# Performance work log

Hardware: AMD Instinct MI355X
Metric: run time of the kernel (lower is better)

## Reference

```python
import jax, jax.numpy as jnp
import numpy as np
from jax import lax

N, D = 16384, 512
E_SPEC, E_SHARED = 8, 2


def setup_inputs() -> dict:
    key = jax.random.key(0)
    ks = jax.random.split(key, 7)
    return {
        "x": jax.random.normal(ks[0], (N, D), dtype=jnp.float32),
        "spec_router_logits": jax.random.normal(ks[1], (N, E_SPEC), dtype=jnp.float32),
        "shared_router_logits": jax.random.normal(ks[2], (N, E_SHARED), dtype=jnp.float32),
        "spec_W": jax.random.normal(ks[3], (E_SPEC, D, D), dtype=jnp.float32) * 0.02,
        "spec_b": jax.random.normal(ks[4], (E_SPEC, D), dtype=jnp.float32) * 0.02,
        "shared_W": jax.random.normal(ks[5], (E_SHARED, D, D), dtype=jnp.float32) * 0.02,
        "shared_b": jax.random.normal(ks[6], (E_SHARED, D), dtype=jnp.float32) * 0.02,
        "top_k": 2,
    }


def reference(x, spec_router_logits, shared_router_logits, spec_W, spec_b, shared_W, shared_b, top_k):
    n, e_spec = spec_router_logits.shape
    # --- specific experts: top-k routing with renormalized weights ---
    spec_probs = jax.nn.softmax(spec_router_logits, axis=1)          # [N, E_spec]
    topk_w, topk_idx = lax.top_k(spec_probs, top_k)                  # [N, K]
    topk_w = topk_w / (jnp.sum(topk_w, axis=1, keepdims=True) + 1e-6)
    # dense per-token per-expert weight matrix (zero for unselected), matching
    # the original dense mask-accumulate loop
    weights = jnp.zeros((n, e_spec), dtype=spec_probs.dtype)
    weights = weights.at[jnp.arange(n)[:, None], topk_idx].add(topk_w)  # [N, E_spec]
    # dense eval of all specific experts (Linear d->d), then weighted combine
    spec_outs = jnp.einsum('nd,edf->enf', x, spec_W) + spec_b[:, None, :]  # [E,N,D]
    spec_out = jnp.einsum('ne,enf->nf', weights, spec_outs)                # [N,D]
    # --- shared experts: soft combine over softmax probs ---
    shared_probs = jax.nn.softmax(shared_router_logits, axis=1)           # [N, E_shared]
    shared_outs = jnp.einsum('nd,edf->enf', x, shared_W) + shared_b[:, None, :]
    shared_out = jnp.einsum('ne,enf->nf', shared_probs, shared_outs)
    return spec_out + shared_out
```

## Files before the change

### kernel.cpp

```cpp
#include <hip/hip_runtime.h>
#include <stdint.h>

typedef unsigned short ushort_t;
typedef __attribute__((ext_vector_type(8))) short short8;
typedef __attribute__((ext_vector_type(4))) float f32x4;
typedef __attribute__((ext_vector_type(4))) unsigned int u32x4;

#define TOK  16384
#define DIM  512
#define NPAIR 64
#define MAXTILES 156

__device__ __forceinline__ unsigned short f2bf(float f) {
  union { float f; uint32_t u; } v; v.f = f;
  uint32_t u = v.u;
  uint32_t r = (u + 0x7fffu + ((u >> 16) & 1u)) >> 16;
  return (unsigned short)r;
}

__global__ void k_prep(const float* __restrict__ wspec, const float* __restrict__ wsh,
                       ushort_t* __restrict__ wt,
                       const float* __restrict__ sl, const float* __restrict__ shl,
                       float* __restrict__ w4, int* __restrict__ pairid,
                       int* __restrict__ cnt) {
  if (blockIdx.z < 10) {
    __shared__ float t[32][33];
    int e = blockIdx.z;
    const float* src = (e < 8) ? (wspec + e * DIM * DIM) : (wsh + (e - 8) * DIM * DIM);
    int tx = threadIdx.x, ty = threadIdx.y;
    int d = blockIdx.y * 32 + ty, f = blockIdx.x * 32 + tx;
    t[ty][tx] = src[d * DIM + f];
    __syncthreads();
    int fo = blockIdx.x * 32 + ty, dd = blockIdx.y * 32 + tx;
    wt[(size_t)e * DIM * DIM + fo * DIM + dd] = f2bf(t[tx][ty]);
    return;
  }
  int blk = blockIdx.y * 16 + blockIdx.x;
  if (blk >= 16) return;
  __shared__ int h[NPAIR];
  int tid = threadIdx.y * 32 + threadIdx.x;
  int n = blk * 1024 + tid;
  if (tid < NPAIR) h[tid] = 0;
  __syncthreads();
  float l[8];
  float m = -1e30f;
#pragma unroll
  for (int i = 0; i < 8; ++i) { l[i] = sl[n*8 + i]; m = fmaxf(m, l[i]); }
  float s = 0.f;
#pragma unroll
  for (int i = 0; i < 8; ++i) { l[i] = expf(l[i] - m); s += l[i]; }
  float inv = 1.f / s;
#pragma unroll
  for (int i = 0; i < 8; ++i) l[i] *= inv;
  int i1 = 0; float v1 = l[0];
#pragma unroll
  for (int i = 1; i < 8; ++i) if (l[i] > v1) { v1 = l[i]; i1 = i; }
  int i2 = -1; float v2 = -1.f;
#pragma unroll
  for (int i = 0; i < 8; ++i) if (i != i1 && l[i] > v2) { v2 = l[i]; i2 = i; }
  float rs = 1.f / (v1 + v2 + 1e-6f);
  float w1 = v1 * rs, w2 = v2 * rs;
  int pmin, pmax; float wa, wb;
  if (i1 < i2) { pmin = i1; pmax = i2; wa = w1; wb = w2; }
  else         { pmin = i2; pmax = i1; wa = w2; wb = w1; }
  float s0 = shl[n*2], s1 = shl[n*2 + 1];
  float mm = fmaxf(s0, s1);
  float e0 = expf(s0 - mm), e1 = expf(s1 - mm);
  float si = 1.f / (e0 + e1);
  w4[n*4 + 0] = wa;
  w4[n*4 + 1] = wb;
  w4[n*4 + 2] = e0 * si;
  w4[n*4 + 3] = e1 * si;
  int p = pmin * 8 + pmax;
  pairid[n] = p;
  atomicAdd(&h[p], 1);
  __syncthreads();
  if (tid < NPAIR && h[tid]) atomicAdd(&cnt[tid], h[tid]);
}

__global__ void k_scan(const int* __restrict__ cnt, int* __restrict__ off,
                       int* __restrict__ cursor, int* __restrict__ tsinfo,
                       int* __restrict__ tileinfo, ushort_t* __restrict__ idx) {
  int l = threadIdx.x;
  int c = cnt[l];
  int t = (c + 127) >> 7;
  int sc = c, st = t;
#pragma unroll
  for (int d = 1; d < 64; d <<= 1) {
    int vc = __shfl_up(sc, d, 64);
    int vt = __shfl_up(st, d, 64);
    if (l >= d) { sc += vc; st += vt; }
  }
  int offv = sc - c, tsv = st - t;
  off[l] = offv; cursor[l] = offv;
  if (l == 63) tsinfo[64] = st;
  for (int q = 0; q < t; ++q) tileinfo[tsv + q] = (l << 16) | q;
  for (int i = l; i < 128; i += 64) idx[TOK + i] = 0;
}

__global__ void k_fill(const int* __restrict__ pairid, int* __restrict__ cursor,
                       ushort_t* __restrict__ idx) {
  __shared__ int hcnt[NPAIR];
  __shared__ int hbase[NPAIR];
  int tid = threadIdx.x;
  int n = blockIdx.x * 256 + tid;
  if (tid < NPAIR) hcnt[tid] = 0;
  __syncthreads();
  int p = pairid[n];
  int r = atomicAdd(&hcnt[p], 1);
  __syncthreads();
  if (tid < NPAIR && hcnt[tid]) hbase[tid] = atomicAdd(&cursor[tid], hcnt[tid]);
  __syncthreads();
  idx[hbase[p] + r] = (ushort_t)n;
}

__global__ void k_gather(const float* __restrict__ x, const ushort_t* __restrict__ idx,
                         ushort_t* __restrict__ xg) {
  int row = blockIdx.x * 4 + (threadIdx.x >> 6);
  int lane = threadIdx.x & 63;
  int t = (int)idx[row];
  const float* src = x + (size_t)t * DIM + lane * 8;
  f32x4 v0 = *(const f32x4*)src;
  f32x4 v1 = *(const f32x4*)(src + 4);
  u32x4 o;
  o[0] = (uint32_t)f2bf(v0[0]) | ((uint32_t)f2bf(v0[1]) << 16);
  o[1] = (uint32_t)f2bf(v0[2]) | ((uint32_t)f2bf(v0[3]) << 16);
  o[2] = (uint32_t)f2bf(v1[0]) | ((uint32_t)f2bf(v1[1]) << 16);
  o[3] = (uint32_t)f2bf(v1[2]) | ((uint32_t)f2bf(v1[3]) << 16);
  *(u32x4*)(xg + (size_t)row * DIM + lane * 8) = o;
}

__global__ __launch_bounds__(256, 3)
void k_moe(const ushort_t* __restrict__ xg, const ushort_t* __restrict__ wt,
           const float* __restrict__ w4, const ushort_t* __restrict__ idx,
           const int* __restrict__ off, const int* __restrict__ cnt,
           const int* __restrict__ tsinfo, const int* __restrict__ tileinfo,
           const float* __restrict__ bspec, const float* __restrict__ bsh,
           float* __restrict__ out) {
  __shared__ ushort_t aB[16384];
  __shared__ ushort_t bB[8192];
  __shared__ float wLT[4 * 128];
  __shared__ float wRT[4 * 128];

  const int tid  = threadIdx.x;
  const int lane = tid & 63;
  const int w    = tid >> 6;
  const int wr   = w >> 1, wc = w & 1;

  int bx  = blockIdx.x;
  int r   = bx >> 3, cdx = bx & 7;
  if (r >= tsinfo[64]) return;
  int info = tileinfo[r];
  int p = info >> 16, tstart = info & 0xffff;
  const int base = off[p] + (tstart << 7);
  int cl = cnt[p] - (tstart << 7); if (cl > 128) cl = 128;
  const int e0 = p >> 3, e1 = p & 7;
  const int tcol = cdx << 6;

  int soffA[8];
#pragma unroll
  for (int q = 0; q < 8; ++q) {
    int pp   = (q << 12) + tid * 16;
    int row  = pp >> 8;
    int orig = (pp & 255) ^ ((row & 7) << 4);
    soffA[q] = row * DIM + (orig >> 1);
  }
  const ushort_t* aSrc = xg + (size_t)base * DIM;
  const ushort_t* bSrc = wt + (size_t)tcol * DIM;

  for (int i = tid; i < 512; i += 256) {
    int j = i >> 7, rs = i & 127;
    float wa = 1.f, wb = 1.f;
    if (rs < cl) {
      int t = (int)idx[base + rs];
      wa = w4[t * 4 + j];
      wb = w4[t * 4 + ((j + 1) & 3)];
    }
    wLT[i] = wa;
    wRT[i] = wa / wb;
  }

  int aRd[4][4], bRd[2][4];
#pragma unroll
  for (int i = 0; i < 4; ++i) {
    int row = wr * 64 + i * 16 + (lane & 15);
#pragma unroll
    for (int ksl = 0; ksl < 4; ++ksl)
      aRd[i][ksl] = row * 256 + ((((ksl << 6) + ((lane >> 4) << 4))) ^ ((row & 7) << 4));
  }
#pragma unroll
  for (int i = 0; i < 2; ++i) {
    int col = wc * 32 + i * 16 + (lane & 15);
#pragma unroll
    for (int ksl = 0; ksl < 4; ++ksl)
      bRd[i][ksl] = col * 256 + ((((ksl << 6) + ((lane >> 4) << 4))) ^ ((col & 7) << 4));
  }

  f32x4 acc[4][2];
#pragma unroll
  for (int a = 0; a < 4; ++a)
#pragma unroll
    for (int b = 0; b < 2; ++b) acc[a][b] = (f32x4){0.f, 0.f, 0.f, 0.f};

#pragma unroll 1
  for (int s = 0; s < 16; ++s) {
    int ks = s >> 2, j = s & 3;
    if (j == 0) {
#pragma unroll
      for (int q = 0; q < 8; ++q)
        __builtin_amdgcn_global_load_lds(
            (const __attribute__((address_space(1))) void*)(aSrc + (ks << 7) + soffA[q]),
            (__attribute__((address_space(3))) void*)((char*)aB + (q << 12) + tid * 16),
            16, 0, 0);
    }
    {
      int e = (j == 0) ? e0 : (j == 1) ? e1 : (j == 2) ? 8 : 9;
      const ushort_t* b = bSrc + ((size_t)e << 18) + (ks << 7);
#pragma unroll
      for (int q = 0; q < 4; ++q)
        __builtin_amdgcn_global_load_lds(
            (const __attribute__((address_space(1))) void*)(b + soffA[q]),
            (__attribute__((address_space(3))) void*)((char*)bB + (q << 12) + tid * 16),
            16, 0, 0);
    }
    __syncthreads();

#pragma unroll
    for (int ksl = 0; ksl < 4; ++ksl) {
      u32x4 af[4], bf[2];
#pragma unroll
      for (int i = 0; i < 4; ++i) af[i] = *(const u32x4*)((const char*)aB + aRd[i][ksl]);
#pragma unroll
      for (int i = 0; i < 2; ++i) bf[i] = *(const u32x4*)((const char*)bB + bRd[i][ksl]);
#pragma unroll
      for (int rb = 0; rb < 4; ++rb) {
        short8 a8 = __builtin_bit_cast(short8, af[rb]);
#pragma unroll
        for (int cb = 0; cb < 2; ++cb) {
          short8 b8 = __builtin_bit_cast(short8, bf[cb]);
          acc[rb][cb] = __builtin_amdgcn_mfma_f32_16x16x32_bf16(a8, b8, acc[rb][cb], 0, 0, 0);
        }
      }
    }

    if (s < 15) {
#pragma unroll
      for (int rb = 0; rb < 4; ++rb) {
        int rl = wr * 64 + rb * 16 + ((lane >> 4) << 2);
        f32x4 rv = *(const f32x4*)&wRT[(j << 7) + rl];
        acc[rb][0] *= rv;
        acc[rb][1] *= rv;
      }
    }
    __syncthreads();
  }

#pragma unroll
  for (int rb = 0; rb < 4; ++rb) {
    int rl = wr * 64 + rb * 16 + ((lane >> 4) << 2);
    f32x4 wv[4];
#pragma unroll
    for (int j = 0; j < 4; ++j) wv[j] = *(const f32x4*)&wLT[(j << 7) + rl];
    int tok[4]; bool pr[4];
#pragma unroll
    for (int q = 0; q < 4; ++q) {
      int rs = rl + q; pr[q] = rs < cl;
      tok[q] = pr[q] ? (int)idx[base + rs] : 0;
    }
#pragma unroll
    for (int cb = 0; cb < 2; ++cb) {
      int cloc = wc * 32 + cb * 16 + (lane & 15);
      f32x4 v = acc[rb][cb] * wv[3];
#pragma unroll
      for (int j = 0; j < 4; ++j) {
        int e = (j == 0) ? e0 : (j == 1) ? e1 : (j == 2) ? 8 : 9;
        float bj = (e < 8) ? bspec[e * DIM + tcol + cloc] : bsh[(e - 8) * DIM + tcol + cloc];
        v += wv[j] * bj;
      }
#pragma unroll
      for (int q = 0; q < 4; ++q)
        if (pr[q]) out[(size_t)tok[q] * DIM + tcol + cloc] = v[q];
    }
  }
}

extern "C" void kernel_launch(void* const* d_in, const int* in_sizes, int n_in,
                              void* d_out, int out_size, void* d_ws, size_t ws_size,
                              hipStream_t stream) {
  (void)in_sizes; (void)n_in; (void)out_size; (void)ws_size;
  const float* x   = (const float*)d_in[0];
  const float* srl = (const float*)d_in[1];
  const float* shl = (const float*)d_in[2];
  const float* sW  = (const float*)d_in[3];
  const float* sb  = (const float*)d_in[4];
  const float* hW  = (const float*)d_in[5];
  const float* hb  = (const float*)d_in[6];
  float* out = (float*)d_out;

  char* ws = (char*)d_ws;
  float*    w4     = (float*)ws;     ws += TOK * 4 * 4;
  int*      pairid = (int*)ws;       ws += TOK * 4;
  ushort_t* idx    = (ushort_t*)ws;  ws += (TOK + 128) * 2 + 256;
  int*      cntp   = (int*)ws;       ws += NPAIR * 4;
  int*      offp   = (int*)ws;       ws += NPAIR * 4;
  int*      curp   = (int*)ws;       ws += NPAIR * 4;
  int*      tsp    = (int*)ws;       ws += (NPAIR + 1) * 4;
  int*      tinfo  = (int*)ws;       ws += MAXTILES * 4 + 208;
  ushort_t* xg     = (ushort_t*)ws;  ws += (size_t)(TOK + 128) * DIM * 2;
  ushort_t* wt     = (ushort_t*)ws;

  hipMemsetAsync(cntp, 0, NPAIR * sizeof(int), stream);
  dim3 tb(32, 32, 1), tg(16, 16, 11);
  k_prep<<<tg, tb, 0, stream>>>(sW, hW, wt, srl, shl, w4, pairid, cntp);
  k_scan<<<1, 64, 0, stream>>>(cntp, offp, curp, tsp, tinfo, idx);
  k_fill<<<TOK / 256, 256, 0, stream>>>(pairid, curp, idx);
  k_gather<<<(TOK + 128) / 4, 256, 0, stream>>>(x, idx, xg);
  k_moe<<<MAXTILES * 8, 256, 0, stream>>>(xg, wt, w4, idx, offp, cntp, tsp, tinfo,
                                          sb, hb, out);
}
```

Baseline: 96.38 us.

## Grow MoE row tiles to 256 tokens with 512-thread blocks and halved K-slab

Doubles the per-tile token count from 128 to 256 and launches 512-thread blocks, so each weight slab staged in LDS is reused by twice as many rows and fewer tiles are needed. The K-slab shrinks from 128 to 64 elements, which doubles the loop to 32 stages and keeps LDS per block roughly constant. Each stage still pays two barriers, so there are more barriers and smaller loads in flight per step. Padding for partially filled 256-row tiles also grows, adding wasted MFMA work per expert pair.

```diff
diff --git a/kernel.cpp b/kernel.cpp
--- a/kernel.cpp
+++ b/kernel.cpp
@@ -9,7 +9,7 @@
 #define TOK  16384
 #define DIM  512
 #define NPAIR 64
-#define MAXTILES 156
+#define MAXT 92
 
 __device__ __forceinline__ unsigned short f2bf(float f) {
   union { float f; uint32_t u; } v; v.f = f;
@@ -83,7 +83,7 @@
                        int* __restrict__ tileinfo, ushort_t* __restrict__ idx) {
   int l = threadIdx.x;
   int c = cnt[l];
-  int t = (c + 127) >> 7;
+  int t = (c + 255) >> 8;
   int sc = c, st = t;
 #pragma unroll
   for (int d = 1; d < 64; d <<= 1) {
@@ -95,7 +95,7 @@
   off[l] = offv; cursor[l] = offv;
   if (l == 63) tsinfo[64] = st;
   for (int q = 0; q < t; ++q) tileinfo[tsv + q] = (l << 16) | q;
-  for (int i = l; i < 128; i += 64) idx[TOK + i] = 0;
+  for (int i = l; i < 256; i += 64) idx[TOK + i] = 0;
 }
 
 __global__ void k_fill(const int* __restrict__ pairid, int* __restrict__ cursor,
@@ -130,7 +130,7 @@
   *(u32x4*)(xg + (size_t)row * DIM + lane * 8) = o;
 }
 
-__global__ __launch_bounds__(256, 3)
+__global__ __launch_bounds__(512, 6)
 void k_moe(const ushort_t* __restrict__ xg, const ushort_t* __restrict__ wt,
            const float* __restrict__ w4, const ushort_t* __restrict__ idx,
            const int* __restrict__ off, const int* __restrict__ cnt,
@@ -138,38 +138,44 @@
            const float* __restrict__ bspec, const float* __restrict__ bsh,
            float* __restrict__ out) {
   __shared__ ushort_t aB[16384];
-  __shared__ ushort_t bB[8192];
-  __shared__ float wLT[4 * 128];
-  __shared__ float wRT[4 * 128];
+  __shared__ ushort_t bB[4096];
+  __shared__ float wLT[4 * 256];
+  __shared__ float wRT[4 * 256];
 
   const int tid  = threadIdx.x;
   const int lane = tid & 63;
   const int w    = tid >> 6;
-  const int wr   = w >> 1, wc = w & 1;
+  const int wr   = w >> 1;
+  const int wc   = w & 1;
 
   int bx  = blockIdx.x;
   int r   = bx >> 3, cdx = bx & 7;
   if (r >= tsinfo[64]) return;
   int info = tileinfo[r];
-  int p = info >> 16, tstart = info & 0xffff;
-  const int base = off[p] + (tstart << 7);
-  int cl = cnt[p] - (tstart << 7); if (cl > 128) cl = 128;
+  int p = info >> 16, tq = info & 0xffff;
+  const int base = off[p] + (tq << 8);
+  int cl = cnt[p] - (tq << 8); if (cl > 256) cl = 256;
   const int e0 = p >> 3, e1 = p & 7;
   const int tcol = cdx << 6;
 
-  int soffA[8];
-#pragma unroll
-  for (int q = 0; q < 8; ++q) {
-    int pp   = (q << 12) + tid * 16;
-    int row  = pp >> 8;
-    int orig = (pp & 255) ^ ((row & 7) << 4);
+  int soffA[4], soffB;
+#pragma unroll
+  for (int q = 0; q < 4; ++q) {
+    int pp   = (q << 13) + tid * 16;
+    int row  = pp >> 7;
+    int orig = (pp & 127) ^ ((row & 7) << 4);
     soffA[q] = row * DIM + (orig >> 1);
+  }
+  {
+    int pp   = tid * 16;
+    int row  = pp >> 7;
+    soffB    = row * DIM + (((pp & 127) ^ ((row & 7) << 4)) >> 1);
   }
   const ushort_t* aSrc = xg + (size_t)base * DIM;
   const ushort_t* bSrc = wt + (size_t)tcol * DIM;
 
-  for (int i = tid; i < 512; i += 256) {
-    int j = i >> 7, rs = i & 127;
+  for (int i = tid; i < 1024; i += 512) {
+    int j = i >> 8, rs = i & 255;
     float wa = 1.f, wb = 1.f;
     if (rs < cl) {
       int t = (int)idx[base + rs];
@@ -180,20 +186,20 @@
     wRT[i] = wa / wb;
   }
 
-  int aRd[4][4], bRd[2][4];
+  int aRd[4][2], bRd[2][2];
 #pragma unroll
   for (int i = 0; i < 4; ++i) {
     int row = wr * 64 + i * 16 + (lane & 15);
 #pragma unroll
-    for (int ksl = 0; ksl < 4; ++ksl)
-      aRd[i][ksl] = row * 256 + ((((ksl << 6) + ((lane >> 4) << 4))) ^ ((row & 7) << 4));
+    for (int ksl = 0; ksl < 2; ++ksl)
+      aRd[i][ksl] = row * 128 + (((ksl << 6) + ((lane >> 4) << 4)) ^ ((row & 7) << 4));
   }
 #pragma unroll
   for (int i = 0; i < 2; ++i) {
     int col = wc * 32 + i * 16 + (lane & 15);
 #pragma unroll
-    for (int ksl = 0; ksl < 4; ++ksl)
-      bRd[i][ksl] = col * 256 + ((((ksl << 6) + ((lane >> 4) << 4))) ^ ((col & 7) << 4));
+    for (int ksl = 0; ksl < 2; ++ksl)
+      bRd[i][ksl] = col * 128 + (((ksl << 6) + ((lane >> 4) << 4)) ^ ((col & 7) << 4));
   }
 
   f32x4 acc[4][2];
@@ -203,30 +209,27 @@
     for (int b = 0; b < 2; ++b) acc[a][b] = (f32x4){0.f, 0.f, 0.f, 0.f};
 
 #pragma unroll 1
-  for (int s = 0; s < 16; ++s) {
+  for (int s = 0; s < 32; ++s) {
     int ks = s >> 2, j = s & 3;
     if (j == 0) {
 #pragma unroll
-      for (int q = 0; q < 8; ++q)
+      for (int q = 0; q < 4; ++q)
         __builtin_amdgcn_global_load_lds(
-            (const __attribute__((address_space(1))) void*)(aSrc + (ks << 7) + soffA[q]),
-            (__attribute__((address_space(3))) void*)((char*)aB + (q << 12) + tid * 16),
+            (const __attribute__((address_space(1))) void*)(aSrc + (ks << 6) + soffA[q]),
+            (__attribute__((address_space(3))) void*)((char*)aB + (q << 13) + tid * 16),
             16, 0, 0);
     }
     {
       int e = (j == 0) ? e0 : (j == 1) ? e1 : (j == 2) ? 8 : 9;
-      const ushort_t* b = bSrc + ((size_t)e << 18) + (ks << 7);
-#pragma unroll
-      for (int q = 0; q < 4; ++q)
-        __builtin_amdgcn_global_load_lds(
-            (const __attribute__((address_space(1))) void*)(b + soffA[q]),
-            (__attribute__((address_space(3))) void*)((char*)bB + (q << 12) + tid * 16),
-            16, 0, 0);
+      __builtin_amdgcn_global_load_lds(
+          (const __attribute__((address_space(1))) void*)(bSrc + ((size_t)e << 18) + (ks << 6) + soffB),
+          (__attribute__((address_space(3))) void*)((char*)bB + tid * 16),
+          16, 0, 0);
     }
     __syncthreads();
 
 #pragma unroll
-    for (int ksl = 0; ksl < 4; ++ksl) {
+    for (int ksl = 0; ksl < 2; ++ksl) {
       u32x4 af[4], bf[2];
 #pragma unroll
       for (int i = 0; i < 4; ++i) af[i] = *(const u32x4*)((const char*)aB + aRd[i][ksl]);
@@ -243,11 +246,11 @@
       }
     }
 
-    if (s < 15) {
+    if (s < 31) {
 #pragma unroll
       for (int rb = 0; rb < 4; ++rb) {
         int rl = wr * 64 + rb * 16 + ((lane >> 4) << 2);
-        f32x4 rv = *(const f32x4*)&wRT[(j << 7) + rl];
+        f32x4 rv = *(const f32x4*)&wRT[(j << 8) + rl];
         acc[rb][0] *= rv;
         acc[rb][1] *= rv;
       }
@@ -260,7 +263,7 @@
     int rl = wr * 64 + rb * 16 + ((lane >> 4) << 2);
     f32x4 wv[4];
 #pragma unroll
-    for (int j = 0; j < 4; ++j) wv[j] = *(const f32x4*)&wLT[(j << 7) + rl];
+    for (int j = 0; j < 4; ++j) wv[j] = *(const f32x4*)&wLT[(j << 8) + rl];
     int tok[4]; bool pr[4];
 #pragma unroll
     for (int q = 0; q < 4; ++q) {
@@ -300,13 +303,13 @@
   char* ws = (char*)d_ws;
   float*    w4     = (float*)ws;     ws += TOK * 4 * 4;
   int*      pairid = (int*)ws;       ws += TOK * 4;
-  ushort_t* idx    = (ushort_t*)ws;  ws += (TOK + 128) * 2 + 256;
+  ushort_t* idx    = (ushort_t*)ws;  ws += (TOK + 256) * 2 + 256;
   int*      cntp   = (int*)ws;       ws += NPAIR * 4;
   int*      offp   = (int*)ws;       ws += NPAIR * 4;
   int*      curp   = (int*)ws;       ws += NPAIR * 4;
   int*      tsp    = (int*)ws;       ws += (NPAIR + 1) * 4;
-  int*      tinfo  = (int*)ws;       ws += MAXTILES * 4 + 208;
-  ushort_t* xg     = (ushort_t*)ws;  ws += (size_t)(TOK + 128) * DIM * 2;
+  int*      tinfo  = (int*)ws;       ws += MAXT * 4 + 208;
+  ushort_t* xg     = (ushort_t*)ws;  ws += (size_t)(TOK + 256) * DIM * 2;
   ushort_t* wt     = (ushort_t*)ws;
 
   hipMemsetAsync(cntp, 0, NPAIR * sizeof(int), stream);
@@ -314,7 +317,7 @@
   k_prep<<<tg, tb, 0, stream>>>(sW, hW, wt, srl, shl, w4, pairid, cntp);
   k_scan<<<1, 64, 0, stream>>>(cntp, offp, curp, tsp, tinfo, idx);
   k_fill<<<TOK / 256, 256, 0, stream>>>(pairid, curp, idx);
-  k_gather<<<(TOK + 128) / 4, 256, 0, stream>>>(x, idx, xg);
-  k_moe<<<MAXTILES * 8, 256, 0, stream>>>(xg, wt, w4, idx, offp, cntp, tsp, tinfo,
-                                          sb, hb, out);
-}
+  k_gather<<<(TOK + 256) / 4, 256, 0, stream>>>(x, idx, xg);
+  k_moe<<<MAXT * 8, 512, 0, stream>>>(xg, wt, w4, idx, offp, cntp, tsp, tinfo,
+                                      sb, hb, out);
+}
```

Result: no change. 97.15 us (+0.8%).
